# Performance work log

Hardware: AMD Instinct MI355X
Metric: run time of the kernel (lower is better)

The kernel has to match this reference:

```python
import jax, jax.numpy as jnp
import numpy as np

S = 1048576   # sequence length (only free scale knob)
D = 20        # d_model (forced == d_internal by the original code)
DI = 20       # d_internal (forced to 20 by output_i[:20])
C = 3         # num_classes
L = 2         # num_layers


def setup_inputs() -> dict:
    key = jax.random.key(0)
    ks = jax.random.split(key, 13)
    f = lambda k, shp, s=1.0: jax.random.normal(k, shp, dtype=jnp.float32) * s
    return {
        "indices": f(ks[0], (S, D)),
        # per-layer stacked parameters (leading axis L)
        "Wq":   f(ks[1], (L, DI, D)),          # torch.randn(d_internal, d)
        "Wk":   f(ks[2], (L, DI, D)),
        "Wv":   f(ks[3], (L, D, D)),           # torch.randn(d, d)
        "Wres": f(ks[4], (L, D, DI)),          # W_residual: (d, d_internal)
        "W1":   f(ks[5], (L, D, DI), 0.2),     # Linear(d_internal, d_model).weight
        "b1":   f(ks[6], (L, D), 0.2),
        "W2":   f(ks[7], (L, D, DI), 0.2),     # second Linear(d_internal, d_model)
        "b2":   f(ks[8], (L, D), 0.2),
        "W3":   f(ks[9], (L, D, D), 0.2),      # Linear(input_dim=d, d_model) residual proj
        "b3":   f(ks[10], (L, D), 0.2),
        "Wc":   f(ks[11], (C, D), 0.2),        # final Linear(d_model, num_classes)
        "bc":   f(ks[12], (C,), 0.2),
    }


def _layer(x, Wq, Wk, Wv, Wres, W1, b1, W2, b2, W3, b3):
    # Vectorized form of the original per-token Python loop.
    q = x @ Wq.T                                   # (S, DI)
    k = x @ Wk.T                                   # (S, DI)
    v = x @ Wv.T                                   # (S, D)
    # scalar similarity per token; softmax over a singleton axis == 1.0 (kept for fidelity)
    sim = jnp.sum(q * k, axis=-1, keepdims=True) / np.sqrt(DI)   # (S, 1)
    p = jax.nn.softmax(sim, axis=-1)               # all ones
    out = (p * v)[:, :DI]                          # output_i = v_i[:20]
    out = out + x @ Wres                           # residual via W_residual
    out = jax.nn.relu(out @ W1.T + b1)             # linear1 + relu
    out = out @ W2.T + b2                          # linear2
    out = out + x @ W3.T + b3                      # final input residual projection
    return out


def reference(indices, Wq, Wk, Wv, Wres, W1, b1, W2, b2, W3, b3, Wc, bc):
    x = indices
    for l in range(L):  # small fixed layer count
        x = _layer(x, Wq[l], Wk[l], Wv[l], Wres[l], W1[l], b1[l], W2[l], b2[l], W3[l], b3[l])
    logits = x @ Wc.T + bc                         # (S, C)
    return jax.nn.softmax(logits, axis=1)
```

## Files before the change

kernel.cpp:

```cpp
#include <hip/hip_runtime.h>
#include <math.h>


#define OFF_G1   0
#define OFF_P1   400
#define OFF_P2   800
#define OFF_Q1   1200
#define OFF_Q2   1280
#define OFF_M2   1360
#define OFF_B11  1440
#define OFF_F2   1460
#define OFF_F3   1480
#define NW       1484
#define OFF_G2   1536
#define OFF_M3   1936
#define OFF_E1   1996

__global__ void prep1_kernel(const float* __restrict__ Wv, const float* __restrict__ Wres,
                             const float* __restrict__ W1, const float* __restrict__ b2,
                             const float* __restrict__ b3, const float* __restrict__ Wc,
                             const float* __restrict__ W3, float* __restrict__ W) {
    const int idx = threadIdx.x;
    if (idx < 400) {
        const int i = idx / 20, m = idx % 20;
        float s = 0.f;
        for (int j = 0; j < 20; ++j)
            s = fmaf(Wv[400 + j*20 + i] + Wres[400 + i*20 + j], W1[400 + m*20 + j], s);
        W[OFF_G2 + idx] = s;
    } else if (idx < 460) {
        const int r = idx - 400, i = r / 3, c = r % 3;
        float s = 0.f;
        for (int p = 0; p < 20; ++p)
            s = fmaf(Wc[c*20 + p], W3[400 + p*20 + i], s);
        W[OFF_M3 + r] = s;
    } else if (idx < 480) {
        const int j = idx - 460;
        W[OFF_E1 + j] = b2[j] + b3[j];
    }
}

__global__ void prep2_kernel(const float* __restrict__ Wv, const float* __restrict__ Wres,
                             const float* __restrict__ W1, const float* __restrict__ b1,
                             const float* __restrict__ W2, const float* __restrict__ b2,
                             const float* __restrict__ b3, const float* __restrict__ Wc,
                             const float* __restrict__ bc, const float* __restrict__ W3,
                             float* __restrict__ W) {
    const float* G2 = W + OFF_G2;
    const float* M3 = W + OFF_M3;
    const float* e1 = W + OFF_E1;
    for (int idx = blockIdx.x * blockDim.x + threadIdx.x; idx < NW; idx += gridDim.x * blockDim.x) {
        float s = 0.f;
        if (idx < 400) {
            const int k = idx / 20, m = idx % 20;
            for (int j = 0; j < 20; ++j)
                s = fmaf(Wv[j*20 + k] + Wres[k*20 + j], W1[m*20 + j], s);
        } else if (idx < 800) {
            const int r = idx - 400, mp = r / 20, m = r % 20;
            for (int i = 0; i < 20; ++i)
                s = fmaf(W2[i*20 + mp], G2[i*20 + m], s);
        } else if (idx < 1200) {
            const int r = idx - 800, k = r / 20, m = r % 20;
            for (int i = 0; i < 20; ++i)
                s = fmaf(W3[i*20 + k], G2[i*20 + m], s);
        } else if (idx < 1280) {
            const int r = idx - 1200, k = r >> 2, c = r & 3;
            if (c < 3)
                for (int i = 0; i < 20; ++i)
                    s = fmaf(W2[i*20 + k], M3[i*3 + c], s);
        } else if (idx < 1360) {
            const int r = idx - 1280, k = r >> 2, c = r & 3;
            if (c < 3)
                for (int i = 0; i < 20; ++i)
                    s = fmaf(W3[i*20 + k], M3[i*3 + c], s);
        } else if (idx < 1440) {
            const int r = idx - 1360, m = r >> 2, c = r & 3;
            if (c < 3)
                for (int p = 0; p < 20; ++p)
                    s = fmaf(Wc[c*20 + p], W2[400 + p*20 + m], s);
        } else if (idx < 1460) {
            s = b1[idx - 1440];
        } else if (idx < 1480) {
            const int m = idx - 1460;
            s = b1[20 + m];
            for (int i = 0; i < 20; ++i)
                s = fmaf(e1[i], G2[i*20 + m], s);
        } else {
            const int c = idx - 1480;
            if (c < 3) {
                s = bc[c];
                for (int p = 0; p < 20; ++p)
                    s = fmaf(Wc[c*20 + p], b2[20 + p] + b3[20 + p], s);
                for (int i = 0; i < 20; ++i)
                    s = fmaf(e1[i], M3[i*3 + c], s);
            }
        }
        W[idx] = s;
    }
}

__global__ __launch_bounds__(256, 2) void fwd_kernel(const float* __restrict__ X,
                                                     const float* __restrict__ Wg,
                                                     float* __restrict__ out, int nquad) {
    __shared__ float Ws[NW];
    for (int i = threadIdx.x; i < NW; i += 256) Ws[i] = Wg[i];
    __syncthreads();

    const int q4 = blockIdx.x * 256 + threadIdx.x;
    if (q4 >= nquad) return;
    const float4* W4 = reinterpret_cast<const float4*>(Ws);
    const float* xbase = X + (size_t)q4 * 80;

    float h[4][20];
    #pragma unroll
    for (int r = 0; r < 5; ++r) {
        const float4 b = W4[OFF_B11/4 + r];
        #pragma unroll
        for (int t = 0; t < 4; ++t) {
            h[t][4*r+0] = b.x; h[t][4*r+1] = b.y; h[t][4*r+2] = b.z; h[t][4*r+3] = b.w;
        }
    }
    #pragma unroll 1
    for (int q = 0; q < 5; ++q) {
        float xr[4][4];
        #pragma unroll
        for (int t = 0; t < 4; ++t) {
            const float4 v = *reinterpret_cast<const float4*>(xbase + t*20 + q*4);
            xr[t][0] = v.x; xr[t][1] = v.y; xr[t][2] = v.z; xr[t][3] = v.w;
        }
        #pragma unroll
        for (int kk = 0; kk < 4; ++kk) {
            const int k = q*4 + kk;
            #pragma unroll
            for (int r = 0; r < 5; ++r) {
                const float4 w = W4[OFF_G1/4 + k*5 + r];
                #pragma unroll
                for (int t = 0; t < 4; ++t) {
                    h[t][4*r+0] = fmaf(xr[t][kk], w.x, h[t][4*r+0]);
                    h[t][4*r+1] = fmaf(xr[t][kk], w.y, h[t][4*r+1]);
                    h[t][4*r+2] = fmaf(xr[t][kk], w.z, h[t][4*r+2]);
                    h[t][4*r+3] = fmaf(xr[t][kk], w.w, h[t][4*r+3]);
                }
            }
        }
    }
    #pragma unroll
    for (int t = 0; t < 4; ++t)
        #pragma unroll
        for (int i = 0; i < 20; ++i) h[t][i] = fmaxf(h[t][i], 0.f);

    float gp[4][20];
    float l[4][3];
    #pragma unroll
    for (int r = 0; r < 5; ++r) {
        const float4 b = W4[OFF_F2/4 + r];
        #pragma unroll
        for (int t = 0; t < 4; ++t) {
            gp[t][4*r+0] = b.x; gp[t][4*r+1] = b.y; gp[t][4*r+2] = b.z; gp[t][4*r+3] = b.w;
        }
    }
    {
        const float4 f3 = W4[OFF_F3/4];
        #pragma unroll
        for (int t = 0; t < 4; ++t) { l[t][0] = f3.x; l[t][1] = f3.y; l[t][2] = f3.z; }
    }
    #pragma unroll
    for (int k = 0; k < 20; ++k) {
        #pragma unroll
        for (int r = 0; r < 5; ++r) {
            const float4 w = W4[OFF_P1/4 + k*5 + r];
            #pragma unroll
            for (int t = 0; t < 4; ++t) {
                gp[t][4*r+0] = fmaf(h[t][k], w.x, gp[t][4*r+0]);
                gp[t][4*r+1] = fmaf(h[t][k], w.y, gp[t][4*r+1]);
                gp[t][4*r+2] = fmaf(h[t][k], w.z, gp[t][4*r+2]);
                gp[t][4*r+3] = fmaf(h[t][k], w.w, gp[t][4*r+3]);
            }
        }
        const float4 wq = W4[OFF_Q1/4 + k];
        #pragma unroll
        for (int t = 0; t < 4; ++t) {
            l[t][0] = fmaf(h[t][k], wq.x, l[t][0]);
            l[t][1] = fmaf(h[t][k], wq.y, l[t][1]);
            l[t][2] = fmaf(h[t][k], wq.z, l[t][2]);
        }
    }

    #pragma unroll 1
    for (int q = 0; q < 5; ++q) {
        float xr[4][4];
        #pragma unroll
        for (int t = 0; t < 4; ++t) {
            const float4 v = *reinterpret_cast<const float4*>(xbase + t*20 + q*4);
            xr[t][0] = v.x; xr[t][1] = v.y; xr[t][2] = v.z; xr[t][3] = v.w;
        }
        #pragma unroll
        for (int kk = 0; kk < 4; ++kk) {
            const int k = q*4 + kk;
            #pragma unroll
            for (int r = 0; r < 5; ++r) {
                const float4 w = W4[OFF_P2/4 + k*5 + r];
                #pragma unroll
                for (int t = 0; t < 4; ++t) {
                    gp[t][4*r+0] = fmaf(xr[t][kk], w.x, gp[t][4*r+0]);
                    gp[t][4*r+1] = fmaf(xr[t][kk], w.y, gp[t][4*r+1]);
                    gp[t][4*r+2] = fmaf(xr[t][kk], w.z, gp[t][4*r+2]);
                    gp[t][4*r+3] = fmaf(xr[t][kk], w.w, gp[t][4*r+3]);
                }
            }
            const float4 wq = W4[OFF_Q2/4 + k];
            #pragma unroll
            for (int t = 0; t < 4; ++t) {
                l[t][0] = fmaf(xr[t][kk], wq.x, l[t][0]);
                l[t][1] = fmaf(xr[t][kk], wq.y, l[t][1]);
                l[t][2] = fmaf(xr[t][kk], wq.z, l[t][2]);
            }
        }
    }

    #pragma unroll
    for (int k = 0; k < 20; ++k) {
        const float4 wm = W4[OFF_M2/4 + k];
        #pragma unroll
        for (int t = 0; t < 4; ++t) {
            const float gk = fmaxf(gp[t][k], 0.f);
            l[t][0] = fmaf(gk, wm.x, l[t][0]);
            l[t][1] = fmaf(gk, wm.y, l[t][1]);
            l[t][2] = fmaf(gk, wm.z, l[t][2]);
        }
    }

    float o[12];
    #pragma unroll
    for (int t = 0; t < 4; ++t) {
        const float m  = fmaxf(fmaxf(l[t][0], l[t][1]), l[t][2]);
        const float e0 = __expf(l[t][0] - m);
        const float e1 = __expf(l[t][1] - m);
        const float e2 = __expf(l[t][2] - m);
        const float r  = 1.f / (e0 + e1 + e2);
        o[3*t+0] = e0 * r; o[3*t+1] = e1 * r; o[3*t+2] = e2 * r;
    }
    float4* o4 = reinterpret_cast<float4*>(out + (size_t)q4 * 12);
    o4[0] = make_float4(o[0], o[1], o[2],  o[3]);
    o4[1] = make_float4(o[4], o[5], o[6],  o[7]);
    o4[2] = make_float4(o[8], o[9], o[10], o[11]);
}

extern "C" void kernel_launch(void* const* d_in, const int* in_sizes, int n_in,
                              void* d_out, int out_size, void* d_ws, size_t ws_size,
                              hipStream_t stream) {
    const float* X    = (const float*)d_in[0];
    const float* Wv   = (const float*)d_in[3];
    const float* Wres = (const float*)d_in[4];
    const float* W1   = (const float*)d_in[5];
    const float* b1   = (const float*)d_in[6];
    const float* W2   = (const float*)d_in[7];
    const float* b2   = (const float*)d_in[8];
    const float* W3   = (const float*)d_in[9];
    const float* b3   = (const float*)d_in[10];
    const float* Wc   = (const float*)d_in[11];
    const float* bc   = (const float*)d_in[12];
    float* out = (float*)d_out;
    float* W   = (float*)d_ws;

    const int S = in_sizes[0] / 20;
    const int nquad = S / 4;

    prep1_kernel<<<1, 512, 0, stream>>>(Wv, Wres, W1, b2, b3, Wc, W3, W);
    prep2_kernel<<<4, 256, 0, stream>>>(Wv, Wres, W1, b1, W2, b2, b3, Wc, bc, W3, W);

    const int block = 256;
    const int grid = (nquad + block - 1) / block;
    fwd_kernel<<<grid, block, 0, stream>>>(X, W, out, nquad);
}
```

Before: 200.8 us.

## Merge prep kernels, preload X into registers, split second layer into halves

The two weight-folding prep kernels become a single one-block kernel that keeps its intermediates in shared memory, removing one launch and a global round trip. The forward kernel loads all 80 input floats per thread into registers before the weight staging, so the global reads overlap the shared-memory fill and X is read only once. The 20-wide second-layer accumulator is split into two halves of 10 (padded to 12), shrinking live registers, and the x/h logit terms are fused into one loop. The bounds check and rounded-up grid are dropped, which assumes S is a multiple of 1024 and holds 80 x values in registers, raising register pressure.

```diff
diff --git a/kernel.cpp b/kernel.cpp
--- a/kernel.cpp
+++ b/kernel.cpp
@@ -3,89 +3,92 @@
 
 
 #define OFF_G1   0
-#define OFF_P1   400
-#define OFF_P2   800
-#define OFF_Q1   1200
-#define OFF_Q2   1280
-#define OFF_M2   1360
-#define OFF_B11  1440
-#define OFF_F2   1460
-#define OFF_F3   1480
-#define NW       1484
-#define OFF_G2   1536
-#define OFF_M3   1936
-#define OFF_E1   1996
-
-__global__ void prep1_kernel(const float* __restrict__ Wv, const float* __restrict__ Wres,
-                             const float* __restrict__ W1, const float* __restrict__ b2,
-                             const float* __restrict__ b3, const float* __restrict__ Wc,
-                             const float* __restrict__ W3, float* __restrict__ W) {
-    const int idx = threadIdx.x;
-    if (idx < 400) {
-        const int i = idx / 20, m = idx % 20;
-        float s = 0.f;
-        for (int j = 0; j < 20; ++j)
-            s = fmaf(Wv[400 + j*20 + i] + Wres[400 + i*20 + j], W1[400 + m*20 + j], s);
-        W[OFF_G2 + idx] = s;
-    } else if (idx < 460) {
-        const int r = idx - 400, i = r / 3, c = r % 3;
-        float s = 0.f;
-        for (int p = 0; p < 20; ++p)
-            s = fmaf(Wc[c*20 + p], W3[400 + p*20 + i], s);
-        W[OFF_M3 + r] = s;
-    } else if (idx < 480) {
-        const int j = idx - 460;
-        W[OFF_E1 + j] = b2[j] + b3[j];
-    }
-}
-
-__global__ void prep2_kernel(const float* __restrict__ Wv, const float* __restrict__ Wres,
-                             const float* __restrict__ W1, const float* __restrict__ b1,
-                             const float* __restrict__ W2, const float* __restrict__ b2,
-                             const float* __restrict__ b3, const float* __restrict__ Wc,
-                             const float* __restrict__ bc, const float* __restrict__ W3,
-                             float* __restrict__ W) {
-    const float* G2 = W + OFF_G2;
-    const float* M3 = W + OFF_M3;
-    const float* e1 = W + OFF_E1;
-    for (int idx = blockIdx.x * blockDim.x + threadIdx.x; idx < NW; idx += gridDim.x * blockDim.x) {
+#define OFF_P1H  400
+#define OFF_P2H  880
+#define OFF_Q1   1360
+#define OFF_Q2   1440
+#define OFF_M2   1520
+#define OFF_B11  1600
+#define OFF_F2H  1620
+#define OFF_F3   1644
+#define NW       1648
+
+__global__ void prep_kernel(const float* __restrict__ Wv, const float* __restrict__ Wres,
+                            const float* __restrict__ W1, const float* __restrict__ b1,
+                            const float* __restrict__ W2, const float* __restrict__ b2,
+                            const float* __restrict__ b3, const float* __restrict__ Wc,
+                            const float* __restrict__ bc, const float* __restrict__ W3,
+                            float* __restrict__ W) {
+    __shared__ float G2[400];
+    __shared__ float M3[60];
+    __shared__ float e1[20];
+    const int tid = threadIdx.x;
+
+    for (int idx = tid; idx < 480; idx += 512) {
+        if (idx < 400) {
+            const int i = idx / 20, m = idx % 20;
+            float s = 0.f;
+            for (int j = 0; j < 20; ++j)
+                s = fmaf(Wv[400 + j*20 + i] + Wres[400 + i*20 + j], W1[400 + m*20 + j], s);
+            G2[idx] = s;
+        } else if (idx < 460) {
+            const int r = idx - 400, i = r / 3, c = r % 3;
+            float s = 0.f;
+            for (int p = 0; p < 20; ++p)
+                s = fmaf(Wc[c*20 + p], W3[400 + p*20 + i], s);
+            M3[r] = s;
+        } else {
+            const int j = idx - 460;
+            e1[j] = b2[j] + b3[j];
+        }
+    }
+    __syncthreads();
+
+    for (int idx = tid; idx < NW; idx += 512) {
         float s = 0.f;
         if (idx < 400) {
             const int k = idx / 20, m = idx % 20;
             for (int j = 0; j < 20; ++j)
                 s = fmaf(Wv[j*20 + k] + Wres[k*20 + j], W1[m*20 + j], s);
-        } else if (idx < 800) {
-            const int r = idx - 400, mp = r / 20, m = r % 20;
-            for (int i = 0; i < 20; ++i)
-                s = fmaf(W2[i*20 + mp], G2[i*20 + m], s);
-        } else if (idx < 1200) {
-            const int r = idx - 800, k = r / 20, m = r % 20;
-            for (int i = 0; i < 20; ++i)
-                s = fmaf(W3[i*20 + k], G2[i*20 + m], s);
-        } else if (idx < 1280) {
-            const int r = idx - 1200, k = r >> 2, c = r & 3;
+        } else if (idx < 880) {
+            const int r = idx - 400, half = r / 240, rr = r % 240;
+            const int k = rr / 12, j = rr % 12, m = 10*half + j;
+            if (j < 10)
+                for (int i = 0; i < 20; ++i)
+                    s = fmaf(W2[i*20 + k], G2[i*20 + m], s);
+        } else if (idx < 1360) {
+            const int r = idx - 880, half = r / 240, rr = r % 240;
+            const int k = rr / 12, j = rr % 12, m = 10*half + j;
+            if (j < 10)
+                for (int i = 0; i < 20; ++i)
+                    s = fmaf(W3[i*20 + k], G2[i*20 + m], s);
+        } else if (idx < 1440) {
+            const int r = idx - 1360, k = r >> 2, c = r & 3;
             if (c < 3)
                 for (int i = 0; i < 20; ++i)
                     s = fmaf(W2[i*20 + k], M3[i*3 + c], s);
-        } else if (idx < 1360) {
-            const int r = idx - 1280, k = r >> 2, c = r & 3;
+        } else if (idx < 1520) {
+            const int r = idx - 1440, k = r >> 2, c = r & 3;
             if (c < 3)
                 for (int i = 0; i < 20; ++i)
                     s = fmaf(W3[i*20 + k], M3[i*3 + c], s);
-        } else if (idx < 1440) {
-            const int r = idx - 1360, m = r >> 2, c = r & 3;
+        } else if (idx < 1600) {
+            const int r = idx - 1520, m = r >> 2, c = r & 3;
             if (c < 3)
                 for (int p = 0; p < 20; ++p)
                     s = fmaf(Wc[c*20 + p], W2[400 + p*20 + m], s);
-        } else if (idx < 1460) {
-            s = b1[idx - 1440];
-        } else if (idx < 1480) {
-            const int m = idx - 1460;
-            s = b1[20 + m];
-            for (int i = 0; i < 20; ++i)
-                s = fmaf(e1[i], G2[i*20 + m], s);
+        } else if (idx < 1620) {
+            s = b1[idx - 1600];
+        } else if (idx < 1644) {
+            const int r = idx - 1620, half = r / 12, j = r % 12;
+            const int m = 10*half + j;
+            if (j < 10) {
+                s = b1[20 + m];
+                for (int i = 0; i < 20; ++i)
+                    s = fmaf(e1[i], G2[i*20 + m], s);
+            }
         } else {
-            const int c = idx - 1480;
+            const int c = idx - 1644;
             if (c < 3) {
                 s = bc[c];
                 for (int p = 0; p < 20; ++p)
@@ -102,13 +105,25 @@
                                                      const float* __restrict__ Wg,
                                                      float* __restrict__ out, int nquad) {
     __shared__ float Ws[NW];
+
+    const int q4 = blockIdx.x * 256 + threadIdx.x;
+
+    float x[4][20];
+    {
+        const float4* xp = reinterpret_cast<const float4*>(X + (size_t)q4 * 80);
+        #pragma unroll
+        for (int t = 0; t < 4; ++t)
+            #pragma unroll
+            for (int q = 0; q < 5; ++q) {
+                const float4 v = xp[t*5 + q];
+                x[t][4*q+0] = v.x; x[t][4*q+1] = v.y;
+                x[t][4*q+2] = v.z; x[t][4*q+3] = v.w;
+            }
+    }
     for (int i = threadIdx.x; i < NW; i += 256) Ws[i] = Wg[i];
     __syncthreads();
 
-    const int q4 = blockIdx.x * 256 + threadIdx.x;
-    if (q4 >= nquad) return;
     const float4* W4 = reinterpret_cast<const float4*>(Ws);
-    const float* xbase = X + (size_t)q4 * 80;
 
     float h[4][20];
     #pragma unroll
@@ -119,113 +134,97 @@
             h[t][4*r+0] = b.x; h[t][4*r+1] = b.y; h[t][4*r+2] = b.z; h[t][4*r+3] = b.w;
         }
     }
+    #pragma unroll
+    for (int k = 0; k < 20; ++k) {
+        #pragma unroll
+        for (int r = 0; r < 5; ++r) {
+            const float4 w = W4[OFF_G1/4 + k*5 + r];
+            #pragma unroll
+            for (int t = 0; t < 4; ++t) {
+                h[t][4*r+0] = fmaf(x[t][k], w.x, h[t][4*r+0]);
+                h[t][4*r+1] = fmaf(x[t][k], w.y, h[t][4*r+1]);
+                h[t][4*r+2] = fmaf(x[t][k], w.z, h[t][4*r+2]);
+                h[t][4*r+3] = fmaf(x[t][k], w.w, h[t][4*r+3]);
+            }
+        }
+    }
+    #pragma unroll
+    for (int t = 0; t < 4; ++t)
+        #pragma unroll
+        for (int i = 0; i < 20; ++i) h[t][i] = fmaxf(h[t][i], 0.f);
+
+    float l[4][3];
+    {
+        const float4 f3 = W4[OFF_F3/4];
+        #pragma unroll
+        for (int t = 0; t < 4; ++t) { l[t][0] = f3.x; l[t][1] = f3.y; l[t][2] = f3.z; }
+    }
+    #pragma unroll
+    for (int k = 0; k < 20; ++k) {
+        const float4 q2 = W4[OFF_Q2/4 + k];
+        const float4 q1 = W4[OFF_Q1/4 + k];
+        #pragma unroll
+        for (int t = 0; t < 4; ++t) {
+            l[t][0] = fmaf(x[t][k], q2.x, l[t][0]);
+            l[t][1] = fmaf(x[t][k], q2.y, l[t][1]);
+            l[t][2] = fmaf(x[t][k], q2.z, l[t][2]);
+            l[t][0] = fmaf(h[t][k], q1.x, l[t][0]);
+            l[t][1] = fmaf(h[t][k], q1.y, l[t][1]);
+            l[t][2] = fmaf(h[t][k], q1.z, l[t][2]);
+        }
+    }
+
     #pragma unroll 1
-    for (int q = 0; q < 5; ++q) {
-        float xr[4][4];
-        #pragma unroll
-        for (int t = 0; t < 4; ++t) {
-            const float4 v = *reinterpret_cast<const float4*>(xbase + t*20 + q*4);
-            xr[t][0] = v.x; xr[t][1] = v.y; xr[t][2] = v.z; xr[t][3] = v.w;
-        }
-        #pragma unroll
-        for (int kk = 0; kk < 4; ++kk) {
-            const int k = q*4 + kk;
-            #pragma unroll
-            for (int r = 0; r < 5; ++r) {
-                const float4 w = W4[OFF_G1/4 + k*5 + r];
+    for (int half = 0; half < 2; ++half) {
+        const int p1b = OFF_P1H/4 + half*60;
+        const int p2b = OFF_P2H/4 + half*60;
+        float gph[4][12];
+        {
+            const float4 f0 = W4[OFF_F2H/4 + half*3 + 0];
+            const float4 f1 = W4[OFF_F2H/4 + half*3 + 1];
+            const float4 f2 = W4[OFF_F2H/4 + half*3 + 2];
+            #pragma unroll
+            for (int t = 0; t < 4; ++t) {
+                gph[t][0] = f0.x; gph[t][1] = f0.y; gph[t][2]  = f0.z; gph[t][3]  = f0.w;
+                gph[t][4] = f1.x; gph[t][5] = f1.y; gph[t][6]  = f1.z; gph[t][7]  = f1.w;
+                gph[t][8] = f2.x; gph[t][9] = f2.y; gph[t][10] = f2.z; gph[t][11] = f2.w;
+            }
+        }
+        #pragma unroll
+        for (int k = 0; k < 20; ++k) {
+            #pragma unroll
+            for (int r = 0; r < 3; ++r) {
+                const float4 w = W4[p2b + k*3 + r];
                 #pragma unroll
                 for (int t = 0; t < 4; ++t) {
-                    h[t][4*r+0] = fmaf(xr[t][kk], w.x, h[t][4*r+0]);
-                    h[t][4*r+1] = fmaf(xr[t][kk], w.y, h[t][4*r+1]);
-                    h[t][4*r+2] = fmaf(xr[t][kk], w.z, h[t][4*r+2]);
-                    h[t][4*r+3] = fmaf(xr[t][kk], w.w, h[t][4*r+3]);
+                    gph[t][4*r+0] = fmaf(x[t][k], w.x, gph[t][4*r+0]);
+                    gph[t][4*r+1] = fmaf(x[t][k], w.y, gph[t][4*r+1]);
+                    gph[t][4*r+2] = fmaf(x[t][k], w.z, gph[t][4*r+2]);
+                    gph[t][4*r+3] = fmaf(x[t][k], w.w, gph[t][4*r+3]);
                 }
             }
-        }
-    }
-    #pragma unroll
-    for (int t = 0; t < 4; ++t)
-        #pragma unroll
-        for (int i = 0; i < 20; ++i) h[t][i] = fmaxf(h[t][i], 0.f);
-
-    float gp[4][20];
-    float l[4][3];
-    #pragma unroll
-    for (int r = 0; r < 5; ++r) {
-        const float4 b = W4[OFF_F2/4 + r];
-        #pragma unroll
-        for (int t = 0; t < 4; ++t) {
-            gp[t][4*r+0] = b.x; gp[t][4*r+1] = b.y; gp[t][4*r+2] = b.z; gp[t][4*r+3] = b.w;
-        }
-    }
-    {
-        const float4 f3 = W4[OFF_F3/4];
-        #pragma unroll
-        for (int t = 0; t < 4; ++t) { l[t][0] = f3.x; l[t][1] = f3.y; l[t][2] = f3.z; }
-    }
-    #pragma unroll
-    for (int k = 0; k < 20; ++k) {
-        #pragma unroll
-        for (int r = 0; r < 5; ++r) {
-            const float4 w = W4[OFF_P1/4 + k*5 + r];
-            #pragma unroll
-            for (int t = 0; t < 4; ++t) {
-                gp[t][4*r+0] = fmaf(h[t][k], w.x, gp[t][4*r+0]);
-                gp[t][4*r+1] = fmaf(h[t][k], w.y, gp[t][4*r+1]);
-                gp[t][4*r+2] = fmaf(h[t][k], w.z, gp[t][4*r+2]);
-                gp[t][4*r+3] = fmaf(h[t][k], w.w, gp[t][4*r+3]);
-            }
-        }
-        const float4 wq = W4[OFF_Q1/4 + k];
-        #pragma unroll
-        for (int t = 0; t < 4; ++t) {
-            l[t][0] = fmaf(h[t][k], wq.x, l[t][0]);
-            l[t][1] = fmaf(h[t][k], wq.y, l[t][1]);
-            l[t][2] = fmaf(h[t][k], wq.z, l[t][2]);
-        }
-    }
-
-    #pragma unroll 1
-    for (int q = 0; q < 5; ++q) {
-        float xr[4][4];
-        #pragma unroll
-        for (int t = 0; t < 4; ++t) {
-            const float4 v = *reinterpret_cast<const float4*>(xbase + t*20 + q*4);
-            xr[t][0] = v.x; xr[t][1] = v.y; xr[t][2] = v.z; xr[t][3] = v.w;
-        }
-        #pragma unroll
-        for (int kk = 0; kk < 4; ++kk) {
-            const int k = q*4 + kk;
-            #pragma unroll
-            for (int r = 0; r < 5; ++r) {
-                const float4 w = W4[OFF_P2/4 + k*5 + r];
+            #pragma unroll
+            for (int r = 0; r < 3; ++r) {
+                const float4 w = W4[p1b + k*3 + r];
                 #pragma unroll
                 for (int t = 0; t < 4; ++t) {
-                    gp[t][4*r+0] = fmaf(xr[t][kk], w.x, gp[t][4*r+0]);
-                    gp[t][4*r+1] = fmaf(xr[t][kk], w.y, gp[t][4*r+1]);
-                    gp[t][4*r+2] = fmaf(xr[t][kk], w.z, gp[t][4*r+2]);
-                    gp[t][4*r+3] = fmaf(xr[t][kk], w.w, gp[t][4*r+3]);
+                    gph[t][4*r+0] = fmaf(h[t][k], w.x, gph[t][4*r+0]);
+                    gph[t][4*r+1] = fmaf(h[t][k], w.y, gph[t][4*r+1]);
+                    gph[t][4*r+2] = fmaf(h[t][k], w.z, gph[t][4*r+2]);
+                    gph[t][4*r+3] = fmaf(h[t][k], w.w, gph[t][4*r+3]);
                 }
             }
-            const float4 wq = W4[OFF_Q2/4 + k];
+        }
+        #pragma unroll
+        for (int m = 0; m < 10; ++m) {
+            const float4 wm = W4[OFF_M2/4 + half*10 + m];
             #pragma unroll
             for (int t = 0; t < 4; ++t) {
-                l[t][0] = fmaf(xr[t][kk], wq.x, l[t][0]);
-                l[t][1] = fmaf(xr[t][kk], wq.y, l[t][1]);
-                l[t][2] = fmaf(xr[t][kk], wq.z, l[t][2]);
-            }
-        }
-    }
-
-    #pragma unroll
-    for (int k = 0; k < 20; ++k) {
-        const float4 wm = W4[OFF_M2/4 + k];
-        #pragma unroll
-        for (int t = 0; t < 4; ++t) {
-            const float gk = fmaxf(gp[t][k], 0.f);
-            l[t][0] = fmaf(gk, wm.x, l[t][0]);
-            l[t][1] = fmaf(gk, wm.y, l[t][1]);
-            l[t][2] = fmaf(gk, wm.z, l[t][2]);
+                const float g = fmaxf(gph[t][m], 0.f);
+                l[t][0] = fmaf(g, wm.x, l[t][0]);
+                l[t][1] = fmaf(g, wm.y, l[t][1]);
+                l[t][2] = fmaf(g, wm.z, l[t][2]);
+            }
         }
     }
 
@@ -265,10 +264,8 @@
     const int S = in_sizes[0] / 20;
     const int nquad = S / 4;
 
-    prep1_kernel<<<1, 512, 0, stream>>>(Wv, Wres, W1, b2, b3, Wc, W3, W);
-    prep2_kernel<<<4, 256, 0, stream>>>(Wv, Wres, W1, b1, W2, b2, b3, Wc, bc, W3, W);
-
-    const int block = 256;
-    const int grid = (nquad + block - 1) / block;
-    fwd_kernel<<<grid, block, 0, stream>>>(X, W, out, nquad);
+    prep_kernel<<<1, 512, 0, stream>>>(Wv, Wres, W1, b1, W2, b2, b3, Wc, bc, W3, W);
+
+    const int grid = nquad / 256;
+    fwd_kernel<<<grid, 256, 0, stream>>>(X, W, out, nquad);
 }
```

Result: slower. 248.4 us (+23.8%).

## Fuse weight-folding prep kernels into forward kernel and merge X passes

Applied to the files above, without the earlier changes.

Removes the two prep kernel launches by having every block recompute the folded weight matrices directly into shared memory before processing tokens. It also merges the two passes over X into a single loop that accumulates the first-layer hidden state and the second-layer X projection together, so each X element is read once. The bounds check and grid rounding are dropped, which assumes the sequence length is a multiple of 1024. The trade-off is redundant per-block prep work: about 1484 dot products of length 20 per block, with global weight reads in every block, plus higher register pressure from keeping h and gp live at the same time.

```diff
diff --git a/kernel.cpp b/kernel.cpp
--- a/kernel.cpp
+++ b/kernel.cpp
@@ -12,52 +12,51 @@
 #define OFF_F2   1460
 #define OFF_F3   1480
 #define NW       1484
-#define OFF_G2   1536
-#define OFF_M3   1936
-#define OFF_E1   1996
-
-__global__ void prep1_kernel(const float* __restrict__ Wv, const float* __restrict__ Wres,
-                             const float* __restrict__ W1, const float* __restrict__ b2,
-                             const float* __restrict__ b3, const float* __restrict__ Wc,
-                             const float* __restrict__ W3, float* __restrict__ W) {
-    const int idx = threadIdx.x;
-    if (idx < 400) {
-        const int i = idx / 20, m = idx % 20;
-        float s = 0.f;
-        for (int j = 0; j < 20; ++j)
-            s = fmaf(Wv[400 + j*20 + i] + Wres[400 + i*20 + j], W1[400 + m*20 + j], s);
-        W[OFF_G2 + idx] = s;
-    } else if (idx < 460) {
-        const int r = idx - 400, i = r / 3, c = r % 3;
-        float s = 0.f;
-        for (int p = 0; p < 20; ++p)
-            s = fmaf(Wc[c*20 + p], W3[400 + p*20 + i], s);
-        W[OFF_M3 + r] = s;
-    } else if (idx < 480) {
-        const int j = idx - 460;
-        W[OFF_E1 + j] = b2[j] + b3[j];
-    }
-}
-
-__global__ void prep2_kernel(const float* __restrict__ Wv, const float* __restrict__ Wres,
-                             const float* __restrict__ W1, const float* __restrict__ b1,
-                             const float* __restrict__ W2, const float* __restrict__ b2,
-                             const float* __restrict__ b3, const float* __restrict__ Wc,
-                             const float* __restrict__ bc, const float* __restrict__ W3,
-                             float* __restrict__ W) {
-    const float* G2 = W + OFF_G2;
-    const float* M3 = W + OFF_M3;
-    const float* e1 = W + OFF_E1;
-    for (int idx = blockIdx.x * blockDim.x + threadIdx.x; idx < NW; idx += gridDim.x * blockDim.x) {
+
+__global__ __launch_bounds__(256, 2) void fused_kernel(
+        const float* __restrict__ X,
+        const float* __restrict__ Wv, const float* __restrict__ Wres,
+        const float* __restrict__ W1, const float* __restrict__ b1,
+        const float* __restrict__ W2, const float* __restrict__ b2,
+        const float* __restrict__ b3, const float* __restrict__ Wc,
+        const float* __restrict__ bc, const float* __restrict__ W3,
+        float* __restrict__ out, int nquad) {
+    __shared__ float Ws[NW];
+    __shared__ float G2[400];
+    __shared__ float M3[60];
+    __shared__ float e1[20];
+    const int tid = threadIdx.x;
+
+    for (int idx = tid; idx < 480; idx += 256) {
+        if (idx < 400) {
+            const int i = idx / 20, m = idx % 20;
+            float s = 0.f;
+            for (int j = 0; j < 20; ++j)
+                s = fmaf(Wv[400 + j*20 + i] + Wres[400 + i*20 + j], W1[400 + m*20 + j], s);
+            G2[idx] = s;
+        } else if (idx < 460) {
+            const int r = idx - 400, i = r / 3, c = r % 3;
+            float s = 0.f;
+            for (int p = 0; p < 20; ++p)
+                s = fmaf(Wc[c*20 + p], W3[400 + p*20 + i], s);
+            M3[r] = s;
+        } else {
+            const int j = idx - 460;
+            e1[j] = b2[j] + b3[j];
+        }
+    }
+    __syncthreads();
+
+    for (int idx = tid; idx < NW; idx += 256) {
         float s = 0.f;
         if (idx < 400) {
             const int k = idx / 20, m = idx % 20;
             for (int j = 0; j < 20; ++j)
                 s = fmaf(Wv[j*20 + k] + Wres[k*20 + j], W1[m*20 + j], s);
         } else if (idx < 800) {
-            const int r = idx - 400, mp = r / 20, m = r % 20;
+            const int r = idx - 400, k = r / 20, m = r % 20;
             for (int i = 0; i < 20; ++i)
-                s = fmaf(W2[i*20 + mp], G2[i*20 + m], s);
+                s = fmaf(W2[i*20 + k], G2[i*20 + m], s);
         } else if (idx < 1200) {
             const int r = idx - 800, k = r / 20, m = r % 20;
             for (int i = 0; i < 20; ++i)
@@ -94,32 +93,32 @@
                     s = fmaf(e1[i], M3[i*3 + c], s);
             }
         }
-        W[idx] = s;
-    }
-}
-
-__global__ __launch_bounds__(256, 2) void fwd_kernel(const float* __restrict__ X,
-                                                     const float* __restrict__ Wg,
-                                                     float* __restrict__ out, int nquad) {
-    __shared__ float Ws[NW];
-    for (int i = threadIdx.x; i < NW; i += 256) Ws[i] = Wg[i];
+        Ws[idx] = s;
+    }
     __syncthreads();
 
-    const int q4 = blockIdx.x * 256 + threadIdx.x;
-    if (q4 >= nquad) return;
     const float4* W4 = reinterpret_cast<const float4*>(Ws);
+    const int q4 = blockIdx.x * 256 + tid;
     const float* xbase = X + (size_t)q4 * 80;
 
-    float h[4][20];
+    float h[4][20], gp[4][20], l[4][3];
     #pragma unroll
     for (int r = 0; r < 5; ++r) {
         const float4 b = W4[OFF_B11/4 + r];
-        #pragma unroll
-        for (int t = 0; t < 4; ++t) {
-            h[t][4*r+0] = b.x; h[t][4*r+1] = b.y; h[t][4*r+2] = b.z; h[t][4*r+3] = b.w;
-        }
-    }
-    #pragma unroll 1
+        const float4 f = W4[OFF_F2/4 + r];
+        #pragma unroll
+        for (int t = 0; t < 4; ++t) {
+            h[t][4*r+0]  = b.x; h[t][4*r+1]  = b.y; h[t][4*r+2]  = b.z; h[t][4*r+3]  = b.w;
+            gp[t][4*r+0] = f.x; gp[t][4*r+1] = f.y; gp[t][4*r+2] = f.z; gp[t][4*r+3] = f.w;
+        }
+    }
+    {
+        const float4 f3 = W4[OFF_F3/4];
+        #pragma unroll
+        for (int t = 0; t < 4; ++t) { l[t][0] = f3.x; l[t][1] = f3.y; l[t][2] = f3.z; }
+    }
+
+    #pragma unroll
     for (int q = 0; q < 5; ++q) {
         float xr[4][4];
         #pragma unroll
@@ -141,61 +140,6 @@
                     h[t][4*r+3] = fmaf(xr[t][kk], w.w, h[t][4*r+3]);
                 }
             }
-        }
-    }
-    #pragma unroll
-    for (int t = 0; t < 4; ++t)
-        #pragma unroll
-        for (int i = 0; i < 20; ++i) h[t][i] = fmaxf(h[t][i], 0.f);
-
-    float gp[4][20];
-    float l[4][3];
-    #pragma unroll
-    for (int r = 0; r < 5; ++r) {
-        const float4 b = W4[OFF_F2/4 + r];
-        #pragma unroll
-        for (int t = 0; t < 4; ++t) {
-            gp[t][4*r+0] = b.x; gp[t][4*r+1] = b.y; gp[t][4*r+2] = b.z; gp[t][4*r+3] = b.w;
-        }
-    }
-    {
-        const float4 f3 = W4[OFF_F3/4];
-        #pragma unroll
-        for (int t = 0; t < 4; ++t) { l[t][0] = f3.x; l[t][1] = f3.y; l[t][2] = f3.z; }
-    }
-    #pragma unroll
-    for (int k = 0; k < 20; ++k) {
-        #pragma unroll
-        for (int r = 0; r < 5; ++r) {
-            const float4 w = W4[OFF_P1/4 + k*5 + r];
-            #pragma unroll
-            for (int t = 0; t < 4; ++t) {
-                gp[t][4*r+0] = fmaf(h[t][k], w.x, gp[t][4*r+0]);
-                gp[t][4*r+1] = fmaf(h[t][k], w.y, gp[t][4*r+1]);
-                gp[t][4*r+2] = fmaf(h[t][k], w.z, gp[t][4*r+2]);
-                gp[t][4*r+3] = fmaf(h[t][k], w.w, gp[t][4*r+3]);
-            }
-        }
-        const float4 wq = W4[OFF_Q1/4 + k];
-        #pragma unroll
-        for (int t = 0; t < 4; ++t) {
-            l[t][0] = fmaf(h[t][k], wq.x, l[t][0]);
-            l[t][1] = fmaf(h[t][k], wq.y, l[t][1]);
-            l[t][2] = fmaf(h[t][k], wq.z, l[t][2]);
-        }
-    }
-
-    #pragma unroll 1
-    for (int q = 0; q < 5; ++q) {
-        float xr[4][4];
-        #pragma unroll
-        for (int t = 0; t < 4; ++t) {
-            const float4 v = *reinterpret_cast<const float4*>(xbase + t*20 + q*4);
-            xr[t][0] = v.x; xr[t][1] = v.y; xr[t][2] = v.z; xr[t][3] = v.w;
-        }
-        #pragma unroll
-        for (int kk = 0; kk < 4; ++kk) {
-            const int k = q*4 + kk;
             #pragma unroll
             for (int r = 0; r < 5; ++r) {
                 const float4 w = W4[OFF_P2/4 + k*5 + r];
@@ -207,25 +151,54 @@
                     gp[t][4*r+3] = fmaf(xr[t][kk], w.w, gp[t][4*r+3]);
                 }
             }
-            const float4 wq = W4[OFF_Q2/4 + k];
+            {
+                const float4 wq = W4[OFF_Q2/4 + k];
+                #pragma unroll
+                for (int t = 0; t < 4; ++t) {
+                    l[t][0] = fmaf(xr[t][kk], wq.x, l[t][0]);
+                    l[t][1] = fmaf(xr[t][kk], wq.y, l[t][1]);
+                    l[t][2] = fmaf(xr[t][kk], wq.z, l[t][2]);
+                }
+            }
+        }
+    }
+
+    #pragma unroll
+    for (int t = 0; t < 4; ++t)
+        #pragma unroll
+        for (int i = 0; i < 20; ++i) h[t][i] = fmaxf(h[t][i], 0.f);
+
+    #pragma unroll
+    for (int k = 0; k < 20; ++k) {
+        #pragma unroll
+        for (int r = 0; r < 5; ++r) {
+            const float4 w = W4[OFF_P1/4 + k*5 + r];
             #pragma unroll
             for (int t = 0; t < 4; ++t) {
-                l[t][0] = fmaf(xr[t][kk], wq.x, l[t][0]);
-                l[t][1] = fmaf(xr[t][kk], wq.y, l[t][1]);
-                l[t][2] = fmaf(xr[t][kk], wq.z, l[t][2]);
-            }
-        }
-    }
-
-    #pragma unroll
-    for (int k = 0; k < 20; ++k) {
-        const float4 wm = W4[OFF_M2/4 + k];
-        #pragma unroll
-        for (int t = 0; t < 4; ++t) {
-            const float gk = fmaxf(gp[t][k], 0.f);
-            l[t][0] = fmaf(gk, wm.x, l[t][0]);
-            l[t][1] = fmaf(gk, wm.y, l[t][1]);
-            l[t][2] = fmaf(gk, wm.z, l[t][2]);
+                gp[t][4*r+0] = fmaf(h[t][k], w.x, gp[t][4*r+0]);
+                gp[t][4*r+1] = fmaf(h[t][k], w.y, gp[t][4*r+1]);
+                gp[t][4*r+2] = fmaf(h[t][k], w.z, gp[t][4*r+2]);
+                gp[t][4*r+3] = fmaf(h[t][k], w.w, gp[t][4*r+3]);
+            }
+        }
+        const float4 wq = W4[OFF_Q1/4 + k];
+        #pragma unroll
+        for (int t = 0; t < 4; ++t) {
+            l[t][0] = fmaf(h[t][k], wq.x, l[t][0]);
+            l[t][1] = fmaf(h[t][k], wq.y, l[t][1]);
+            l[t][2] = fmaf(h[t][k], wq.z, l[t][2]);
+        }
+    }
+
+    #pragma unroll
+    for (int m = 0; m < 20; ++m) {
+        const float4 wm = W4[OFF_M2/4 + m];
+        #pragma unroll
+        for (int t = 0; t < 4; ++t) {
+            const float g = fmaxf(gp[t][m], 0.f);
+            l[t][0] = fmaf(g, wm.x, l[t][0]);
+            l[t][1] = fmaf(g, wm.y, l[t][1]);
+            l[t][2] = fmaf(g, wm.z, l[t][2]);
         }
     }
 
@@ -260,15 +233,11 @@
     const float* Wc   = (const float*)d_in[11];
     const float* bc   = (const float*)d_in[12];
     float* out = (float*)d_out;
-    float* W   = (float*)d_ws;
 
     const int S = in_sizes[0] / 20;
     const int nquad = S / 4;
-
-    prep1_kernel<<<1, 512, 0, stream>>>(Wv, Wres, W1, b2, b3, Wc, W3, W);
-    prep2_kernel<<<4, 256, 0, stream>>>(Wv, Wres, W1, b1, W2, b2, b3, Wc, bc, W3, W);
-
-    const int block = 256;
-    const int grid = (nquad + block - 1) / block;
-    fwd_kernel<<<grid, block, 0, stream>>>(X, W, out, nquad);
+    const int grid = nquad / 256;
+
+    fused_kernel<<<grid, 256, 0, stream>>>(X, Wv, Wres, W1, b1, W2, b2, b3,
+                                           Wc, bc, W3, out, nquad);
 }
```

New measurement: 184.7 us. -8.0%, faster.
